# Performance work log

Hardware: AMD Instinct MI355X
Metric: run time of the kernel (lower is better)

The kernel has to match this reference:

```python
import jax, jax.numpy as jnp
import numpy as np

N_NODES = 40000
N_EDGES = 640000
NODE_D = 128
EDGE_D = 64
OUT_D = 128


def setup_inputs() -> dict:
    key = jax.random.key(0)
    ks = jax.random.split(key, 8)
    return {
        "node_features": jax.random.normal(ks[0], (N_NODES, NODE_D), dtype=jnp.float32),
        "edge_features": jax.random.normal(ks[1], (N_EDGES, EDGE_D), dtype=jnp.float32),
        "src": jax.random.randint(ks[2], (N_EDGES,), 0, N_NODES, dtype=jnp.int32),
        "dst": jax.random.randint(ks[3], (N_EDGES,), 0, N_NODES, dtype=jnp.int32),
        "W_msg_w": jax.random.normal(ks[4], (OUT_D, NODE_D + EDGE_D), dtype=jnp.float32) * 0.05,
        "W_msg_b": jax.random.normal(ks[5], (OUT_D,), dtype=jnp.float32) * 0.05,
        "W_apply_w": jax.random.normal(ks[6], (OUT_D, OUT_D + NODE_D), dtype=jnp.float32) * 0.05,
        "W_apply_b": jax.random.normal(ks[7], (OUT_D,), dtype=jnp.float32) * 0.05,
    }


def reference(node_features, edge_features, src, dst, W_msg_w, W_msg_b, W_apply_w, W_apply_b):
    n_nodes = node_features.shape[0]
    # message: gather src node feats, concat edge feats, linear + relu  [E, OUT_D]
    msg_in = jnp.concatenate([node_features[src], edge_features], axis=-1)
    m = jax.nn.relu(msg_in @ W_msg_w.T + W_msg_b)
    # aggregate: sum messages into destination nodes  [N, OUT_D]
    h_neigh = jax.ops.segment_sum(m, dst, num_segments=n_nodes)
    # apply: concat original node feats with aggregated messages, linear + relu
    apply_in = jnp.concatenate([node_features, h_neigh], axis=-1)
    return jax.nn.relu(apply_in @ W_apply_w.T + W_apply_b)
```

## Files before the change

kernel.cpp:

```cpp
#include <hip/hip_runtime.h>
#include <hip/hip_bf16.h>
#include <stdint.h>

#define NN 40000
#define NE 640000
#define ND 128
#define ED 64
#define OD 128
#define KM 192
#define KA 256
#define NB 40

typedef __attribute__((ext_vector_type(8))) short bf16x8;
typedef __attribute__((ext_vector_type(4))) float f32x4;
typedef __attribute__((ext_vector_type(4))) unsigned short us4;

__device__ __forceinline__ uint32_t pkbf2(float a, float b) {
    __hip_bfloat162 h = __float22bfloat162_rn(make_float2(a, b));
    union { __hip_bfloat162 h; uint32_t u; } cv; cv.h = h; return cv.u;
}
__device__ __forceinline__ unsigned short f2bf1(float f) {
    __hip_bfloat16 h = __float2bfloat16(f);
    union { __hip_bfloat16 h; unsigned short u; } cv; cv.h = h; return cv.u;
}
__device__ __forceinline__ us4 pk4(float4 v) {
    union { uint2 u; us4 s; } cv;
    cv.u.x = pkbf2(v.x, v.y);
    cv.u.y = pkbf2(v.z, v.w);
    return cv.s;
}
__device__ __forceinline__ bf16x8 pk8(float4 a, float4 b) {
    union { uint4 u; bf16x8 s; } cv;
    cv.u.x = pkbf2(a.x, a.y); cv.u.y = pkbf2(a.z, a.w);
    cv.u.z = pkbf2(b.x, b.y); cv.u.w = pkbf2(b.z, b.w);
    return cv.s;
}
__device__ __forceinline__ void st_bf4(unsigned short* p, float4 v) {
    uint2 r; r.x = pkbf2(v.x, v.y); r.y = pkbf2(v.z, v.w);
    *(uint2*)p = r;
}
__device__ __forceinline__ float b2f(unsigned short u) {
    union { uint32_t u; float f; } v; v.u = ((uint32_t)u) << 16; return v.f;
}

__global__ void hist_kernel(const int* __restrict__ dst, int* __restrict__ cnt) {
    int e = blockIdx.x * blockDim.x + threadIdx.x;
    if (e < NE) atomicAdd(&cnt[dst[e]], 1);
}

__global__ __launch_bounds__(1024) void scanA_kernel(
    int* __restrict__ cur, int* __restrict__ bsum)
{
    __shared__ int wsum[16];
    const int t = threadIdx.x, b = blockIdx.x;
    const int idx = b * 1024 + t;
    int v = (idx < NN) ? cur[idx] : 0;
    int x = v;
    #pragma unroll
    for (int d = 1; d < 64; d <<= 1) {
        int y = __shfl_up(x, d, 64);
        if ((t & 63) >= d) x += y;
    }
    const int wid = t >> 6;
    if ((t & 63) == 63) wsum[wid] = x;
    __syncthreads();
    if (t < 16) {
        int s = wsum[t];
        #pragma unroll
        for (int d = 1; d < 16; d <<= 1) {
            int y = __shfl_up(s, d, 64);
            if (t >= d) s += y;
        }
        wsum[t] = s;
    }
    __syncthreads();
    int incl = x + (wid > 0 ? wsum[wid - 1] : 0);
    if (idx < NN) cur[idx] = incl - v;
    if (t == 1023) bsum[b] = incl;
}

__global__ __launch_bounds__(1024) void scanC_kernel(
    int* __restrict__ cur, const int* __restrict__ bsum)
{
    __shared__ int sboff;
    const int t = threadIdx.x, b = blockIdx.x;
    if (t < 64) {
        int v = (t < b) ? bsum[t] : 0;
        #pragma unroll
        for (int d = 32; d > 0; d >>= 1) v += __shfl_down(v, d, 64);
        if (t == 0) sboff = v;
    }
    __syncthreads();
    const int idx = b * 1024 + t;
    if (idx < NN) cur[idx] += sboff;
}

__global__ void scatter_kernel(const int* __restrict__ dst, const int* __restrict__ src,
                               int* __restrict__ cur, int4* __restrict__ tri) {
    int e = blockIdx.x * blockDim.x + threadIdx.x;
    if (e < NE) {
        int s = src[e];
        int d = dst[e];
        int p = atomicAdd(&cur[d], 1);
        tri[p] = make_int4(e, s, d, 0);
    }
}

#define PT 32
__global__ __launch_bounds__(256, 2) void proj_kernel(
    const float* __restrict__ node, const float* __restrict__ Wm,
    unsigned short* __restrict__ P)
{
    __shared__ unsigned short sW[OD][136];
    __shared__ unsigned short sA[PT][136];
    const int t = threadIdx.x, n0 = blockIdx.x * PT;
    {
        int el = t >> 3, sub = t & 7;
        const float* np = node + (size_t)(n0 + el) * ND + sub * 16;
        #pragma unroll
        for (int i = 0; i < 4; ++i) {
            float4 v = *(const float4*)(np + i * 4);
            *(us4*)&sA[el][sub * 16 + i * 4] = pk4(v);
        }
    }
    for (int i = t; i < OD * 128 / 4; i += 256) {
        int base = i * 4;
        int n = base / 128, k = base % 128;
        float4 wv = *(const float4*)(Wm + n * KM + k);
        *(us4*)&sW[n][k] = pk4(wv);
    }
    __syncthreads();

    const int w = t >> 6, lane = t & 63, l15 = lane & 15, lhi = lane >> 4;
    const int koff = lhi * 8;
    f32x4 acc[2][2] = {};
    #pragma unroll
    for (int ks = 0; ks < 4; ++ks) {
        bf16x8 a0 = *(const bf16x8*)&sA[l15][ks * 32 + koff];
        bf16x8 a1 = *(const bf16x8*)&sA[16 + l15][ks * 32 + koff];
        bf16x8 b0 = *(const bf16x8*)&sW[w * 32 + l15][ks * 32 + koff];
        bf16x8 b1 = *(const bf16x8*)&sW[w * 32 + 16 + l15][ks * 32 + koff];
        acc[0][0] = __builtin_amdgcn_mfma_f32_16x16x32_bf16(a0, b0, acc[0][0], 0, 0, 0);
        acc[1][0] = __builtin_amdgcn_mfma_f32_16x16x32_bf16(a1, b0, acc[1][0], 0, 0, 0);
        acc[0][1] = __builtin_amdgcn_mfma_f32_16x16x32_bf16(a0, b1, acc[0][1], 0, 0, 0);
        acc[1][1] = __builtin_amdgcn_mfma_f32_16x16x32_bf16(a1, b1, acc[1][1], 0, 0, 0);
    }
    #pragma unroll
    for (int ai = 0; ai < 2; ++ai)
        #pragma unroll
        for (int r = 0; r < 4; ++r) {
            int m = n0 + ai * 16 + 4 * lhi + r;
            #pragma unroll
            for (int bj = 0; bj < 2; ++bj) {
                int n = w * 32 + bj * 16 + l15;
                P[(size_t)m * OD + n] = f2bf1(acc[ai][bj][r]);
            }
        }
}

#define QT 64
#define MROW 148
#define GRID_MSG 2048

__global__ __launch_bounds__(256, 4) void msgagg_kernel(
    const float* __restrict__ edgef, const int4* __restrict__ tri,
    const unsigned short* __restrict__ P,
    const float* __restrict__ Wm, const float* __restrict__ bm,
    float* __restrict__ hn)
{
    __shared__ union {
        struct {
            unsigned short E[QT][72];
            unsigned short Pp[QT][136];
        } s;
        unsigned short m[QT][MROW];
    } u;
    __shared__ int sD[QT];

    const int t = threadIdx.x;
    const int w = t >> 6, lane = t & 63, l15 = lane & 15, lhi = lane >> 4;
    const int row = t >> 2, s4 = t & 3;

    bf16x8 bw[2][2];
    #pragma unroll
    for (int bj = 0; bj < 2; ++bj) {
        int n = w * 32 + bj * 16 + l15;
        const float* wp = Wm + n * KM + ND;
        #pragma unroll
        for (int ks = 0; ks < 2; ++ks) {
            float4 x = *(const float4*)(wp + ks * 32 + lhi * 8);
            float4 y = *(const float4*)(wp + ks * 32 + lhi * 8 + 4);
            bw[ks][bj] = pk8(x, y);
        }
    }
    float bmv[2] = { bm[w * 32 + l15], bm[w * 32 + 16 + l15] };

    const int NT = NE / QT;
    int tile = blockIdx.x;
    if (tile >= NT) return;

    float4 rE0, rE1, rE2, rE3;
    uint4  rP0, rP1, rP2, rP3;
    int4 id, idn;

#define GATHER() do { \
        const float* ep_ = edgef + (size_t)id.x * ED + s4 * 16; \
        rE0 = *(const float4*)(ep_ + 0); \
        rE1 = *(const float4*)(ep_ + 4); \
        rE2 = *(const float4*)(ep_ + 8); \
        rE3 = *(const float4*)(ep_ + 12); \
        const uint4* pp_ = (const uint4*)(P + (size_t)id.y * OD) + s4 * 4; \
        rP0 = pp_[0]; rP1 = pp_[1]; rP2 = pp_[2]; rP3 = pp_[3]; \
    } while (0)

    id = tri[(size_t)tile * QT + row];
    GATHER();
    {
        int nx = tile + GRID_MSG;
        idn = tri[(size_t)(nx < NT ? nx : 0) * QT + row];
    }

    for (;;) {
        st_bf4(&u.s.E[row][s4 * 16 +  0], rE0);
        st_bf4(&u.s.E[row][s4 * 16 +  4], rE1);
        st_bf4(&u.s.E[row][s4 * 16 +  8], rE2);
        st_bf4(&u.s.E[row][s4 * 16 + 12], rE3);
        *(uint4*)&u.s.Pp[row][s4 * 32 +  0] = rP0;
        *(uint4*)&u.s.Pp[row][s4 * 32 +  8] = rP1;
        *(uint4*)&u.s.Pp[row][s4 * 32 + 16] = rP2;
        *(uint4*)&u.s.Pp[row][s4 * 32 + 24] = rP3;
        if (s4 == 0) sD[row] = id.z;
        __syncthreads();

        const int next = tile + GRID_MSG;
        const bool more = next < NT;
        if (more) {
            id = idn;
            GATHER();
            int nx2 = next + GRID_MSG;
            idn = tri[(size_t)(nx2 < NT ? nx2 : 0) * QT + row];
        }

        f32x4 acc[4][2] = {};
        #pragma unroll
        for (int ks = 0; ks < 2; ++ks) {
            bf16x8 a[4];
            #pragma unroll
            for (int ai = 0; ai < 4; ++ai)
                a[ai] = *(const bf16x8*)&u.s.E[ai * 16 + l15][ks * 32 + lhi * 8];
            #pragma unroll
            for (int ai = 0; ai < 4; ++ai) {
                acc[ai][0] = __builtin_amdgcn_mfma_f32_16x16x32_bf16(a[ai], bw[ks][0], acc[ai][0], 0, 0, 0);
                acc[ai][1] = __builtin_amdgcn_mfma_f32_16x16x32_bf16(a[ai], bw[ks][1], acc[ai][1], 0, 0, 0);
            }
        }

        #pragma unroll
        for (int ai = 0; ai < 4; ++ai)
            #pragma unroll
            for (int r = 0; r < 4; ++r) {
                int m = ai * 16 + 4 * lhi + r;
                #pragma unroll
                for (int bj = 0; bj < 2; ++bj) {
                    int n = w * 32 + bj * 16 + l15;
                    float v = acc[ai][bj][r] + bmv[bj] + b2f(u.s.Pp[m][n]);
                    acc[ai][bj][r] = v > 0.f ? v : 0.f;
                }
            }
        __syncthreads();

        #pragma unroll
        for (int ai = 0; ai < 4; ++ai)
            #pragma unroll
            for (int r = 0; r < 4; ++r) {
                int m = ai * 16 + 4 * lhi + r;
                #pragma unroll
                for (int bj = 0; bj < 2; ++bj) {
                    int n = w * 32 + bj * 16 + l15;
                    u.m[m][n] = f2bf1(acc[ai][bj][r]);
                }
            }
        __syncthreads();

        {
            const int half = t >> 7;
            const int c = t & 127;
            const int r0 = half * 32;
            int dprev = sD[r0];
            int start = r0;
            float accv = b2f(u.m[r0][c]);
            #pragma unroll 8
            for (int r = r0 + 1; r < r0 + 32; ++r) {
                int d = sD[r];
                float v = b2f(u.m[r][c]);
                if (d != dprev) {
                    float* dest = hn + (size_t)dprev * OD + c;
                    if (start > r0) *dest = accv;
                    else atomicAdd(dest, accv);
                    accv = v; dprev = d; start = r;
                } else {
                    accv += v;
                }
            }
            float* dest = hn + (size_t)dprev * OD + c;
            bool cont = (half == 0) ? (sD[32] == dprev) : true;
            if (!cont && start > r0) *dest = accv;
            else atomicAdd(dest, accv);
        }

        if (!more) break;
        tile = next;
        __syncthreads();
    }
#undef GATHER
}

#define MT 32
#define LK (KM + 8)
__global__ __launch_bounds__(256, 2) void msg_kernel_atomic(
    const float* __restrict__ node, const float* __restrict__ edgef,
    const int* __restrict__ src, const int* __restrict__ dst,
    const float* __restrict__ Wm, const float* __restrict__ bm,
    float* __restrict__ hn)
{
    __shared__ unsigned short sW[OD][LK];
    __shared__ unsigned short sA[MT][LK];

    const int t  = threadIdx.x;
    const int e0 = blockIdx.x * MT;

    for (int i = t; i < OD * KM / 4; i += 256) {
        int base = i * 4;
        int n = base / KM, k = base % KM;
        float4 w = *(const float4*)(Wm + n * KM + k);
        *(us4*)&sW[n][k] = pk4(w);
    }
    {
        int el = t >> 3, sub = t & 7;
        int s = src[e0 + el];
        const float* np = node + (size_t)s * ND + sub * 16;
        #pragma unroll
        for (int i = 0; i < 4; ++i) {
            float4 v = *(const float4*)(np + i * 4);
            *(us4*)&sA[el][sub * 16 + i * 4] = pk4(v);
        }
        const float* ep = edgef + (size_t)(e0 + el) * ED + sub * 8;
        #pragma unroll
        for (int i = 0; i < 2; ++i) {
            float4 v = *(const float4*)(ep + i * 4);
            *(us4*)&sA[el][ND + sub * 8 + i * 4] = pk4(v);
        }
    }
    __syncthreads();

    const int w = t >> 6, lane = t & 63, l15 = lane & 15, lhi = lane >> 4;
    const int koff = lhi * 8;
    f32x4 acc[2][2] = {};

    #pragma unroll
    for (int ks = 0; ks < 6; ++ks) {
        bf16x8 a0 = *(const bf16x8*)&sA[l15][ks * 32 + koff];
        bf16x8 a1 = *(const bf16x8*)&sA[16 + l15][ks * 32 + koff];
        bf16x8 b0 = *(const bf16x8*)&sW[w * 32 + l15][ks * 32 + koff];
        bf16x8 b1 = *(const bf16x8*)&sW[w * 32 + 16 + l15][ks * 32 + koff];
        acc[0][0] = __builtin_amdgcn_mfma_f32_16x16x32_bf16(a0, b0, acc[0][0], 0, 0, 0);
        acc[1][0] = __builtin_amdgcn_mfma_f32_16x16x32_bf16(a1, b0, acc[1][0], 0, 0, 0);
        acc[0][1] = __builtin_amdgcn_mfma_f32_16x16x32_bf16(a0, b1, acc[0][1], 0, 0, 0);
        acc[1][1] = __builtin_amdgcn_mfma_f32_16x16x32_bf16(a1, b1, acc[1][1], 0, 0, 0);
    }

    #pragma unroll
    for (int ai = 0; ai < 2; ++ai)
        #pragma unroll
        for (int r = 0; r < 4; ++r) {
            int el = ai * 16 + 4 * lhi + r;
            int d  = dst[e0 + el];
            float* hrow = hn + (size_t)d * OD;
            #pragma unroll
            for (int bj = 0; bj < 2; ++bj) {
                int n = w * 32 + bj * 16 + l15;
                float v = acc[ai][bj][r] + bm[n];
                v = v > 0.f ? v : 0.f;
                atomicAdd(hrow + n, v);
            }
        }
}

#define AT 32
#define LKA (KA + 8)
#define LKW (128 + 8)

__global__ __launch_bounds__(256, 2) void apply_kernel(
    const float* __restrict__ node, const float* __restrict__ hn,
    const float* __restrict__ Wa, const float* __restrict__ ba,
    float* __restrict__ out)
{
    __shared__ unsigned short sW[OD][LKW];
    __shared__ unsigned short sA[AT][LKA];

    const int t  = threadIdx.x;
    const int n0 = blockIdx.x * AT;

    {
        int el = t >> 3, sub = t & 7;
        const float* np = node + (size_t)(n0 + el) * ND + sub * 16;
        #pragma unroll
        for (int i = 0; i < 4; ++i) {
            float4 v = *(const float4*)(np + i * 4);
            *(us4*)&sA[el][sub * 16 + i * 4] = pk4(v);
        }
        const float* hp = hn + (size_t)(n0 + el) * OD + sub * 16;
        #pragma unroll
        for (int i = 0; i < 4; ++i) {
            float4 v = *(const float4*)(hp + i * 4);
            *(us4*)&sA[el][ND + sub * 16 + i * 4] = pk4(v);
        }
    }
    for (int i = t; i < OD * 128 / 4; i += 256) {
        int base = i * 4;
        int n = base / 128, k = base % 128;
        float4 w = *(const float4*)(Wa + n * KA + k);
        *(us4*)&sW[n][k] = pk4(w);
    }
    __syncthreads();

    const int w = t >> 6, lane = t & 63, l15 = lane & 15, lhi = lane >> 4;
    const int koff = lhi * 8;
    f32x4 acc[2][2] = {};

    #pragma unroll
    for (int ks = 0; ks < 4; ++ks) {
        bf16x8 a0 = *(const bf16x8*)&sA[l15][ks * 32 + koff];
        bf16x8 a1 = *(const bf16x8*)&sA[16 + l15][ks * 32 + koff];
        bf16x8 b0 = *(const bf16x8*)&sW[w * 32 + l15][ks * 32 + koff];
        bf16x8 b1 = *(const bf16x8*)&sW[w * 32 + 16 + l15][ks * 32 + koff];
        acc[0][0] = __builtin_amdgcn_mfma_f32_16x16x32_bf16(a0, b0, acc[0][0], 0, 0, 0);
        acc[1][0] = __builtin_amdgcn_mfma_f32_16x16x32_bf16(a1, b0, acc[1][0], 0, 0, 0);
        acc[0][1] = __builtin_amdgcn_mfma_f32_16x16x32_bf16(a0, b1, acc[0][1], 0, 0, 0);
        acc[1][1] = __builtin_amdgcn_mfma_f32_16x16x32_bf16(a1, b1, acc[1][1], 0, 0, 0);
    }
    __syncthreads();
    for (int i = t; i < OD * 128 / 4; i += 256) {
        int base = i * 4;
        int n = base / 128, k = base % 128;
        float4 w = *(const float4*)(Wa + n * KA + 128 + k);
        *(us4*)&sW[n][k] = pk4(w);
    }
    __syncthreads();
    #pragma unroll
    for (int ks = 0; ks < 4; ++ks) {
        bf16x8 a0 = *(const bf16x8*)&sA[l15][128 + ks * 32 + koff];
        bf16x8 a1 = *(const bf16x8*)&sA[16 + l15][128 + ks * 32 + koff];
        bf16x8 b0 = *(const bf16x8*)&sW[w * 32 + l15][ks * 32 + koff];
        bf16x8 b1 = *(const bf16x8*)&sW[w * 32 + 16 + l15][ks * 32 + koff];
        acc[0][0] = __builtin_amdgcn_mfma_f32_16x16x32_bf16(a0, b0, acc[0][0], 0, 0, 0);
        acc[1][0] = __builtin_amdgcn_mfma_f32_16x16x32_bf16(a1, b0, acc[1][0], 0, 0, 0);
        acc[0][1] = __builtin_amdgcn_mfma_f32_16x16x32_bf16(a0, b1, acc[0][1], 0, 0, 0);
        acc[1][1] = __builtin_amdgcn_mfma_f32_16x16x32_bf16(a1, b1, acc[1][1], 0, 0, 0);
    }

    #pragma unroll
    for (int ai = 0; ai < 2; ++ai)
        #pragma unroll
        for (int r = 0; r < 4; ++r) {
            int nd = n0 + ai * 16 + 4 * lhi + r;
            #pragma unroll
            for (int bj = 0; bj < 2; ++bj) {
                int n = w * 32 + bj * 16 + l15;
                float v = acc[ai][bj][r] + ba[n];
                out[(size_t)nd * OD + n] = v > 0.f ? v : 0.f;
            }
        }
}

extern "C" void kernel_launch(void* const* d_in, const int* in_sizes, int n_in,
                              void* d_out, int out_size, void* d_ws, size_t ws_size,
                              hipStream_t stream) {
    const float* node  = (const float*)d_in[0];
    const float* edgef = (const float*)d_in[1];
    const int*   src   = (const int*)d_in[2];
    const int*   dst   = (const int*)d_in[3];
    const float* Wm    = (const float*)d_in[4];
    const float* bm    = (const float*)d_in[5];
    const float* Wa    = (const float*)d_in[6];
    const float* ba    = (const float*)d_in[7];
    float* out = (float*)d_out;

    size_t o = 0;
    const size_t o_P    = o; o += (size_t)NN * OD * 2;
    const size_t o_hn   = o; o += (size_t)NN * OD * 4;
    const size_t o_tri  = o; o += (size_t)NE * 16;
    const size_t o_cur  = o; o += (size_t)NN * 4;
    const size_t o_bsum = o; o += 64 * 4;
    const size_t need   = o;

    char* ws = (char*)d_ws;

    if (ws_size >= need) {
        unsigned short* P  = (unsigned short*)(ws + o_P);
        float* hn   = (float*)(ws + o_hn);
        int4*  tri  = (int4*)(ws + o_tri);
        int*   cur  = (int*)(ws + o_cur);
        int*   bsum = (int*)(ws + o_bsum);

        hipMemsetAsync(cur, 0, (size_t)NN * 4, stream);
        hipMemsetAsync(hn, 0, (size_t)NN * OD * 4, stream);
        hist_kernel<<<(NE + 255) / 256, 256, 0, stream>>>(dst, cur);
        scanA_kernel<<<NB, 1024, 0, stream>>>(cur, bsum);
        scanC_kernel<<<NB, 1024, 0, stream>>>(cur, bsum);
        scatter_kernel<<<(NE + 255) / 256, 256, 0, stream>>>(dst, src, cur, tri);
        proj_kernel<<<NN / PT, 256, 0, stream>>>(node, Wm, P);
        msgagg_kernel<<<GRID_MSG, 256, 0, stream>>>(edgef, tri, P, Wm, bm, hn);
        apply_kernel<<<NN / AT, 256, 0, stream>>>(node, hn, Wa, ba, out);
    } else {
        const size_t hn_bytes = (size_t)NN * OD * 4;
        float* hn = (ws_size >= hn_bytes) ? (float*)d_ws : out;
        hipMemsetAsync(hn, 0, hn_bytes, stream);
        msg_kernel_atomic<<<NE / MT, 256, 0, stream>>>(node, edgef, src, dst, Wm, bm, hn);
        apply_kernel<<<NN / AT, 256, 0, stream>>>(node, hn, Wa, ba, out);
    }
}
```

Before: 213.9 us.

## Pre-sort edge features into bf16 buffer during scatter, streamline msgagg gathers

The scatter pass now also reads each edge's fp32 features, converts them to bf16 and writes them into a dst-sorted buffer. It also writes compact (src,dst) pairs in place of int4 triples. The message kernel then reads edge features contiguously by tile instead of gathering them randomly in fp32, and it skips the conversion step. This costs an extra full pass that writes bf16 edge features. The grid also grows to 2500 with occupancy 5, which may pressure registers.

```diff
diff --git a/kernel.cpp b/kernel.cpp
--- a/kernel.cpp
+++ b/kernel.cpp
@@ -35,10 +35,6 @@
     cv.u.z = pkbf2(b.x, b.y); cv.u.w = pkbf2(b.z, b.w);
     return cv.s;
 }
-__device__ __forceinline__ void st_bf4(unsigned short* p, float4 v) {
-    uint2 r; r.x = pkbf2(v.x, v.y); r.y = pkbf2(v.z, v.w);
-    *(uint2*)p = r;
-}
 __device__ __forceinline__ float b2f(unsigned short u) {
     union { uint32_t u; float f; } v; v.u = ((uint32_t)u) << 16; return v.f;
 }
@@ -95,15 +91,35 @@
     if (idx < NN) cur[idx] += sboff;
 }
 
-__global__ void scatter_kernel(const int* __restrict__ dst, const int* __restrict__ src,
-                               int* __restrict__ cur, int4* __restrict__ tri) {
-    int e = blockIdx.x * blockDim.x + threadIdx.x;
-    if (e < NE) {
-        int s = src[e];
-        int d = dst[e];
-        int p = atomicAdd(&cur[d], 1);
-        tri[p] = make_int4(e, s, d, 0);
-    }
+__global__ __launch_bounds__(256) void scatter2_kernel(
+    const int* __restrict__ src, const int* __restrict__ dst,
+    const float* __restrict__ edgef,
+    int* __restrict__ cur, int2* __restrict__ sd, uint4* __restrict__ eb)
+{
+    const int t = blockIdx.x * blockDim.x + threadIdx.x;
+    const int e  = t >> 2;
+    const int s4 = t & 3;
+    if (e >= NE) return;
+    const int lane = threadIdx.x & 63;
+
+    int d = dst[e];
+    int p = 0;
+    if (s4 == 0) p = atomicAdd(&cur[d], 1);
+    p = __shfl(p, lane & ~3, 64);
+    if (s4 == 0) sd[p] = make_int2(src[e], d);
+
+    const float* ep = edgef + (size_t)e * ED + s4 * 16;
+    float4 a = *(const float4*)(ep + 0);
+    float4 b = *(const float4*)(ep + 4);
+    float4 c = *(const float4*)(ep + 8);
+    float4 g = *(const float4*)(ep + 12);
+    uint4 w0, w1;
+    w0.x = pkbf2(a.x, a.y); w0.y = pkbf2(a.z, a.w);
+    w0.z = pkbf2(b.x, b.y); w0.w = pkbf2(b.z, b.w);
+    w1.x = pkbf2(c.x, c.y); w1.y = pkbf2(c.z, c.w);
+    w1.z = pkbf2(g.x, g.y); w1.w = pkbf2(g.z, g.w);
+    eb[(size_t)p * 8 + s4 * 2 + 0] = w0;
+    eb[(size_t)p * 8 + s4 * 2 + 1] = w1;
 }
 
 #define PT 32
@@ -160,10 +176,10 @@
 
 #define QT 64
 #define MROW 148
-#define GRID_MSG 2048
-
-__global__ __launch_bounds__(256, 4) void msgagg_kernel(
-    const float* __restrict__ edgef, const int4* __restrict__ tri,
+#define GRID_MSG 2500
+
+__global__ __launch_bounds__(256, 5) void msgagg_kernel(
+    const uint4* __restrict__ eb, const int2* __restrict__ sd,
     const unsigned short* __restrict__ P,
     const float* __restrict__ Wm, const float* __restrict__ bm,
     float* __restrict__ hn)
@@ -199,46 +215,42 @@
     int tile = blockIdx.x;
     if (tile >= NT) return;
 
-    float4 rE0, rE1, rE2, rE3;
-    uint4  rP0, rP1, rP2, rP3;
-    int4 id, idn;
+    uint4 rE0, rE1, rP0, rP1, rP2, rP3;
+    int2 id, idn;
 
 #define GATHER() do { \
-        const float* ep_ = edgef + (size_t)id.x * ED + s4 * 16; \
-        rE0 = *(const float4*)(ep_ + 0); \
-        rE1 = *(const float4*)(ep_ + 4); \
-        rE2 = *(const float4*)(ep_ + 8); \
-        rE3 = *(const float4*)(ep_ + 12); \
-        const uint4* pp_ = (const uint4*)(P + (size_t)id.y * OD) + s4 * 4; \
+        rE0 = eb[(size_t)tile_g * 512 + t * 2 + 0]; \
+        rE1 = eb[(size_t)tile_g * 512 + t * 2 + 1]; \
+        const uint4* pp_ = (const uint4*)(P + (size_t)id.x * OD) + s4 * 4; \
         rP0 = pp_[0]; rP1 = pp_[1]; rP2 = pp_[2]; rP3 = pp_[3]; \
     } while (0)
 
-    id = tri[(size_t)tile * QT + row];
-    GATHER();
     {
+        int tile_g = tile;
+        id = sd[(size_t)tile * QT + row];
+        GATHER();
         int nx = tile + GRID_MSG;
-        idn = tri[(size_t)(nx < NT ? nx : 0) * QT + row];
+        idn = sd[(size_t)(nx < NT ? nx : 0) * QT + row];
     }
 
     for (;;) {
-        st_bf4(&u.s.E[row][s4 * 16 +  0], rE0);
-        st_bf4(&u.s.E[row][s4 * 16 +  4], rE1);
-        st_bf4(&u.s.E[row][s4 * 16 +  8], rE2);
-        st_bf4(&u.s.E[row][s4 * 16 + 12], rE3);
+        *(uint4*)&u.s.E[row][s4 * 16 + 0] = rE0;
+        *(uint4*)&u.s.E[row][s4 * 16 + 8] = rE1;
         *(uint4*)&u.s.Pp[row][s4 * 32 +  0] = rP0;
         *(uint4*)&u.s.Pp[row][s4 * 32 +  8] = rP1;
         *(uint4*)&u.s.Pp[row][s4 * 32 + 16] = rP2;
         *(uint4*)&u.s.Pp[row][s4 * 32 + 24] = rP3;
-        if (s4 == 0) sD[row] = id.z;
+        if (s4 == 0) sD[row] = id.y;
         __syncthreads();
 
         const int next = tile + GRID_MSG;
         const bool more = next < NT;
         if (more) {
+            int tile_g = next;
             id = idn;
             GATHER();
             int nx2 = next + GRID_MSG;
-            idn = tri[(size_t)(nx2 < NT ? nx2 : 0) * QT + row];
+            idn = sd[(size_t)(nx2 < NT ? nx2 : 0) * QT + row];
         }
 
         f32x4 acc[4][2] = {};
@@ -489,7 +501,8 @@
     size_t o = 0;
     const size_t o_P    = o; o += (size_t)NN * OD * 2;
     const size_t o_hn   = o; o += (size_t)NN * OD * 4;
-    const size_t o_tri  = o; o += (size_t)NE * 16;
+    const size_t o_eb   = o; o += (size_t)NE * ED * 2;
+    const size_t o_sd   = o; o += (size_t)NE * 8;
     const size_t o_cur  = o; o += (size_t)NN * 4;
     const size_t o_bsum = o; o += 64 * 4;
     const size_t need   = o;
@@ -499,7 +512,8 @@
     if (ws_size >= need) {
         unsigned short* P  = (unsigned short*)(ws + o_P);
         float* hn   = (float*)(ws + o_hn);
-        int4*  tri  = (int4*)(ws + o_tri);
+        uint4* eb   = (uint4*)(ws + o_eb);
+        int2*  sd   = (int2*)(ws + o_sd);
         int*   cur  = (int*)(ws + o_cur);
         int*   bsum = (int*)(ws + o_bsum);
 
@@ -508,9 +522,9 @@
         hist_kernel<<<(NE + 255) / 256, 256, 0, stream>>>(dst, cur);
         scanA_kernel<<<NB, 1024, 0, stream>>>(cur, bsum);
         scanC_kernel<<<NB, 1024, 0, stream>>>(cur, bsum);
-        scatter_kernel<<<(NE + 255) / 256, 256, 0, stream>>>(dst, src, cur, tri);
         proj_kernel<<<NN / PT, 256, 0, stream>>>(node, Wm, P);
-        msgagg_kernel<<<GRID_MSG, 256, 0, stream>>>(edgef, tri, P, Wm, bm, hn);
+        scatter2_kernel<<<(NE * 4) / 256, 256, 0, stream>>>(src, dst, edgef, cur, sd, eb);
+        msgagg_kernel<<<GRID_MSG, 256, 0, stream>>>(eb, sd, P, Wm, bm, hn);
         apply_kernel<<<NN / AT, 256, 0, stream>>>(node, hn, Wa, ba, out);
     } else {
         const size_t hn_bytes = (size_t)NN * OD * 4;
```

Result: slower. 286.3 us (+33.9%).

## Give each message block a contiguous tile span and carry segment sums across tiles

Applied to the files above, without the earlier changes.

The message/aggregate kernel now handles a contiguous run of four dst-sorted tiles per block instead of a grid-strided set. Per-column segment accumulators carry across tile boundaries, so fewer atomics hit global memory at tile edges, and 128 threads now do the 64-row scan. The bias is folded into the projected node table, and zeroing of the aggregate buffer is merged into the histogram kernel to drop a memset. The cost is a serial 64-row reduction on half the threads, a larger grid with higher occupancy bounds, and extra store bandwidth in the histogram pass.

```diff
diff --git a/kernel.cpp b/kernel.cpp
--- a/kernel.cpp
+++ b/kernel.cpp
@@ -35,17 +35,20 @@
     cv.u.z = pkbf2(b.x, b.y); cv.u.w = pkbf2(b.z, b.w);
     return cv.s;
 }
-__device__ __forceinline__ void st_bf4(unsigned short* p, float4 v) {
-    uint2 r; r.x = pkbf2(v.x, v.y); r.y = pkbf2(v.z, v.w);
-    *(uint2*)p = r;
-}
 __device__ __forceinline__ float b2f(unsigned short u) {
     union { uint32_t u; float f; } v; v.u = ((uint32_t)u) << 16; return v.f;
 }
 
-__global__ void hist_kernel(const int* __restrict__ dst, int* __restrict__ cnt) {
+__global__ __launch_bounds__(256) void hist_kernel(
+    const int* __restrict__ dst, int* __restrict__ cnt, float4* __restrict__ hnz)
+{
     int e = blockIdx.x * blockDim.x + threadIdx.x;
     if (e < NE) atomicAdd(&cnt[dst[e]], 1);
+    #pragma unroll
+    for (int k = 0; k < 2; ++k) {
+        int j = e + k * (NE);
+        if (j < NN * OD / 4) hnz[j] = make_float4(0.f, 0.f, 0.f, 0.f);
+    }
 }
 
 __global__ __launch_bounds__(1024) void scanA_kernel(
@@ -109,7 +112,7 @@
 #define PT 32
 __global__ __launch_bounds__(256, 2) void proj_kernel(
     const float* __restrict__ node, const float* __restrict__ Wm,
-    unsigned short* __restrict__ P)
+    const float* __restrict__ bm, unsigned short* __restrict__ P)
 {
     __shared__ unsigned short sW[OD][136];
     __shared__ unsigned short sA[PT][136];
@@ -133,6 +136,7 @@
 
     const int w = t >> 6, lane = t & 63, l15 = lane & 15, lhi = lane >> 4;
     const int koff = lhi * 8;
+    float bmv[2] = { bm[w * 32 + l15], bm[w * 32 + 16 + l15] };
     f32x4 acc[2][2] = {};
     #pragma unroll
     for (int ks = 0; ks < 4; ++ks) {
@@ -153,19 +157,20 @@
             #pragma unroll
             for (int bj = 0; bj < 2; ++bj) {
                 int n = w * 32 + bj * 16 + l15;
-                P[(size_t)m * OD + n] = f2bf1(acc[ai][bj][r]);
+                P[(size_t)m * OD + n] = f2bf1(acc[ai][bj][r] + bmv[bj]);
             }
         }
 }
 
 #define QT 64
 #define MROW 148
-#define GRID_MSG 2048
-
-__global__ __launch_bounds__(256, 4) void msgagg_kernel(
+#define SPAN 4
+#define GRID_MSG (NE / (QT * SPAN))
+
+__global__ __launch_bounds__(256, 5) void msgagg_kernel(
     const float* __restrict__ edgef, const int4* __restrict__ tri,
     const unsigned short* __restrict__ P,
-    const float* __restrict__ Wm, const float* __restrict__ bm,
+    const float* __restrict__ Wm,
     float* __restrict__ hn)
 {
     __shared__ union {
@@ -193,11 +198,9 @@
             bw[ks][bj] = pk8(x, y);
         }
     }
-    float bmv[2] = { bm[w * 32 + l15], bm[w * 32 + 16 + l15] };
-
-    const int NT = NE / QT;
-    int tile = blockIdx.x;
-    if (tile >= NT) return;
+
+    const int tile0 = blockIdx.x * SPAN;
+    const int tend  = tile0 + SPAN;
 
     float4 rE0, rE1, rE2, rE3;
     uint4  rP0, rP1, rP2, rP3;
@@ -213,18 +216,27 @@
         rP0 = pp_[0]; rP1 = pp_[1]; rP2 = pp_[2]; rP3 = pp_[3]; \
     } while (0)
 
-    id = tri[(size_t)tile * QT + row];
+    id = tri[(size_t)tile0 * QT + row];
     GATHER();
-    {
-        int nx = tile + GRID_MSG;
-        idn = tri[(size_t)(nx < NT ? nx : 0) * QT + row];
-    }
-
-    for (;;) {
-        st_bf4(&u.s.E[row][s4 * 16 +  0], rE0);
-        st_bf4(&u.s.E[row][s4 * 16 +  4], rE1);
-        st_bf4(&u.s.E[row][s4 * 16 +  8], rE2);
-        st_bf4(&u.s.E[row][s4 * 16 + 12], rE3);
+    idn = tri[(size_t)(tile0 + 1 < tend ? tile0 + 1 : tile0) * QT + row];
+
+    float accv = 0.f;
+    int   dprev = -1;
+    bool  started = false;
+    const int c = t & 127;
+
+    for (int tile = tile0; tile < tend; ++tile) {
+        {
+            st4: ;
+            uint2 e0; e0.x = pkbf2(rE0.x, rE0.y); e0.y = pkbf2(rE0.z, rE0.w);
+            uint2 e1; e1.x = pkbf2(rE1.x, rE1.y); e1.y = pkbf2(rE1.z, rE1.w);
+            uint2 e2; e2.x = pkbf2(rE2.x, rE2.y); e2.y = pkbf2(rE2.z, rE2.w);
+            uint2 e3; e3.x = pkbf2(rE3.x, rE3.y); e3.y = pkbf2(rE3.z, rE3.w);
+            *(uint2*)&u.s.E[row][s4 * 16 +  0] = e0;
+            *(uint2*)&u.s.E[row][s4 * 16 +  4] = e1;
+            *(uint2*)&u.s.E[row][s4 * 16 +  8] = e2;
+            *(uint2*)&u.s.E[row][s4 * 16 + 12] = e3;
+        }
         *(uint4*)&u.s.Pp[row][s4 * 32 +  0] = rP0;
         *(uint4*)&u.s.Pp[row][s4 * 32 +  8] = rP1;
         *(uint4*)&u.s.Pp[row][s4 * 32 + 16] = rP2;
@@ -232,13 +244,12 @@
         if (s4 == 0) sD[row] = id.z;
         __syncthreads();
 
-        const int next = tile + GRID_MSG;
-        const bool more = next < NT;
+        const bool more = (tile + 1) < tend;
         if (more) {
             id = idn;
             GATHER();
-            int nx2 = next + GRID_MSG;
-            idn = tri[(size_t)(nx2 < NT ? nx2 : 0) * QT + row];
+            int nx2 = tile + 2 < tend ? tile + 2 : tile + 1;
+            idn = tri[(size_t)nx2 * QT + row];
         }
 
         f32x4 acc[4][2] = {};
@@ -263,7 +274,7 @@
                 #pragma unroll
                 for (int bj = 0; bj < 2; ++bj) {
                     int n = w * 32 + bj * 16 + l15;
-                    float v = acc[ai][bj][r] + bmv[bj] + b2f(u.s.Pp[m][n]);
+                    float v = acc[ai][bj][r] + b2f(u.s.Pp[m][n]);
                     acc[ai][bj][r] = v > 0.f ? v : 0.f;
                 }
             }
@@ -282,35 +293,31 @@
             }
         __syncthreads();
 
-        {
-            const int half = t >> 7;
-            const int c = t & 127;
-            const int r0 = half * 32;
-            int dprev = sD[r0];
-            int start = r0;
-            float accv = b2f(u.m[r0][c]);
+        if (t < 128) {
             #pragma unroll 8
-            for (int r = r0 + 1; r < r0 + 32; ++r) {
+            for (int r = 0; r < QT; ++r) {
                 int d = sD[r];
                 float v = b2f(u.m[r][c]);
                 if (d != dprev) {
-                    float* dest = hn + (size_t)dprev * OD + c;
-                    if (start > r0) *dest = accv;
-                    else atomicAdd(dest, accv);
-                    accv = v; dprev = d; start = r;
+                    if (dprev >= 0) {
+                        float* dest = hn + (size_t)dprev * OD + c;
+                        if (started) *dest = accv;
+                        else atomicAdd(dest, accv);
+                    }
+                    bool ns = (dprev >= 0);
+                    accv = v; dprev = d; started = ns ? true : started;
+                    if (dprev >= 0 && !ns) started = false;
+                    if (ns) started = true;
                 } else {
                     accv += v;
                 }
             }
-            float* dest = hn + (size_t)dprev * OD + c;
-            bool cont = (half == 0) ? (sD[32] == dprev) : true;
-            if (!cont && start > r0) *dest = accv;
-            else atomicAdd(dest, accv);
-        }
-
-        if (!more) break;
-        tile = next;
+        }
         __syncthreads();
+    }
+
+    if (t < 128 && dprev >= 0) {
+        atomicAdd(hn + (size_t)dprev * OD + c, accv);
     }
 #undef GATHER
 }
@@ -504,13 +511,12 @@
         int*   bsum = (int*)(ws + o_bsum);
 
         hipMemsetAsync(cur, 0, (size_t)NN * 4, stream);
-        hipMemsetAsync(hn, 0, (size_t)NN * OD * 4, stream);
-        hist_kernel<<<(NE + 255) / 256, 256, 0, stream>>>(dst, cur);
+        hist_kernel<<<(NE + 255) / 256, 256, 0, stream>>>(dst, cur, (float4*)hn);
         scanA_kernel<<<NB, 1024, 0, stream>>>(cur, bsum);
         scanC_kernel<<<NB, 1024, 0, stream>>>(cur, bsum);
+        proj_kernel<<<NN / PT, 256, 0, stream>>>(node, Wm, bm, P);
         scatter_kernel<<<(NE + 255) / 256, 256, 0, stream>>>(dst, src, cur, tri);
-        proj_kernel<<<NN / PT, 256, 0, stream>>>(node, Wm, P);
-        msgagg_kernel<<<GRID_MSG, 256, 0, stream>>>(edgef, tri, P, Wm, bm, hn);
+        msgagg_kernel<<<GRID_MSG, 256, 0, stream>>>(edgef, tri, P, Wm, hn);
         apply_kernel<<<NN / AT, 256, 0, stream>>>(node, hn, Wa, ba, out);
     } else {
         const size_t hn_bytes = (size_t)NN * OD * 4;
```

Measured after the change: 225.1 us. 5.3% more time.
